# Optimization experiments

Hardware: AMD Instinct MI355X
Metric: run time of the kernel (lower is better)

The kernel has to match this reference:

```python
import jax, jax.numpy as jnp
import numpy as np

D_MODEL = 1024
D_STATE = 16
D_CONV = 4
EXPAND = 2
D_INNER = EXPAND * D_MODEL
DT_RANK = (D_MODEL + 15) // 16  # ceil(d_model/16) = 64
BATCH = 2
SEQLEN = 1024


def _causal_conv_silu(x, w, b):
    # x: (B, d_inner, L); w: (d_inner, 1, k) depthwise; causal left padding k-1
    k = w.shape[-1]
    y = jax.lax.conv_general_dilated(
        x, w, window_strides=(1,), padding=[(k - 1, 0)],
        dimension_numbers=("NCH", "OIH", "NCH"), feature_group_count=x.shape[1])
    return jax.nn.silu(y + b[None, :, None])


def _ssm_scan(dA, dBx):
    # h_t = dA_t * h_{t-1} + dBx_t, parallel associative scan over L (axis=2)
    def op(e1, e2):
        a1, b1 = e1
        a2, b2 = e2
        return (a1 * a2, a2 * b1 + b2)
    return jax.lax.associative_scan(op, (dA, dBx), axis=2)[1]


def _mamba_dir(xz, conv_w, conv_b, xproj_w, dtproj_w, dt_bias, A_log, Dp):
    d_inner = xz.shape[1] // 2
    x, z = xz[:, :d_inner], xz[:, d_inner:]
    u = _causal_conv_silu(x, conv_w, conv_b)                  # (B, d, L)
    x_dbl = jnp.einsum('bdl,kd->bkl', u, xproj_w)             # (B, dt_rank+2n, L)
    n = A_log.shape[1]
    r = dtproj_w.shape[1]
    delta = jnp.einsum('dr,brl->bdl', dtproj_w, x_dbl[:, :r])
    Bm = x_dbl[:, r:r + n]                                    # (B, n, L)
    Cm = x_dbl[:, r + n:]                                     # (B, n, L)
    delta = jax.nn.softplus(delta + dt_bias[None, :, None])
    A = -jnp.exp(A_log)                                       # (d, n)
    dA = jnp.exp(jnp.einsum('bdl,dn->bdln', delta, A))
    dBx = jnp.einsum('bdl,bnl,bdl->bdln', delta, Bm, u)
    h = _ssm_scan(dA, dBx)                                    # (B, d, L, n)
    y = jnp.einsum('bdln,bnl->bdl', h, Cm)
    y = y + Dp[None, :, None] * u
    return y * jax.nn.silu(z)


def setup_inputs() -> dict:
    key = jax.random.key(0)
    ks = jax.random.split(key, 16)
    s_in = 1.0 / np.sqrt(D_MODEL)
    s_x = 1.0 / np.sqrt(D_INNER)
    dt_std = DT_RANK ** -0.5

    def dt_bias_init(k):
        dt = jnp.exp(jax.random.uniform(k, (D_INNER,)) * (np.log(0.1) - np.log(0.001)) + np.log(0.001))
        dt = jnp.clip(dt, 1e-4, None)
        return dt + jnp.log(-jnp.expm1(-dt))  # inverse softplus

    A_log = jnp.log(jnp.tile(jnp.arange(1, D_STATE + 1, dtype=jnp.float32)[None, :], (D_INNER, 1)))
    inp = {
        'hidden_states': jax.random.normal(ks[0], (BATCH, SEQLEN, D_MODEL), jnp.float32),
        'in_proj_w': jax.random.normal(ks[1], (2 * D_INNER, D_MODEL), jnp.float32) * s_in,
        'conv_w': jax.random.normal(ks[2], (D_INNER, 1, D_CONV), jnp.float32) * 0.3,
        'conv_bias': jnp.zeros((D_INNER,), jnp.float32),
        'x_proj_w': jax.random.normal(ks[3], (DT_RANK + 2 * D_STATE, D_INNER), jnp.float32) * s_x,
        'dt_proj_w': jax.random.uniform(ks[4], (D_INNER, DT_RANK), jnp.float32, -dt_std, dt_std),
        'dt_proj_bias': dt_bias_init(ks[5]),
        'A_log': A_log,
        'D_skip': jnp.ones((D_INNER,), jnp.float32),
        'convb_w': jax.random.normal(ks[6], (D_INNER, 1, D_CONV), jnp.float32) * 0.3,
        'convb_bias': jnp.zeros((D_INNER,), jnp.float32),
        'x_proj_b_w': jax.random.normal(ks[7], (DT_RANK + 2 * D_STATE, D_INNER), jnp.float32) * s_x,
        'dt_proj_b_w': jax.random.uniform(ks[8], (D_INNER, DT_RANK), jnp.float32, -dt_std, dt_std),
        'dt_proj_b_bias': dt_bias_init(ks[9]),
        'A_b_log': A_log,
        'D_b_skip': jnp.ones((D_INNER,), jnp.float32),
        'out_proj_w': jax.random.normal(ks[10], (D_MODEL, D_INNER), jnp.float32) * s_x,
    }
    return inp


def reference(hidden_states, in_proj_w, conv_w, conv_bias, x_proj_w, dt_proj_w,
              dt_proj_bias, A_log, D_skip, convb_w, convb_bias, x_proj_b_w,
              dt_proj_b_w, dt_proj_b_bias, A_b_log, D_b_skip, out_proj_w):
    # in_proj (no bias): (B, 2*d_inner, L)
    xz = jnp.einsum('ed,bld->bel', in_proj_w, hidden_states)
    out_f = _mamba_dir(xz, conv_w, conv_bias, x_proj_w, dt_proj_w, dt_proj_bias, A_log, D_skip)
    out_b = _mamba_dir(xz[:, :, ::-1], convb_w, convb_bias, x_proj_b_w, dt_proj_b_w,
                       dt_proj_b_bias, A_b_log, D_b_skip)[:, :, ::-1]
    # if_divide_out=False: just sum then out_proj (no bias)
    return jnp.einsum('bdl,od->blo', out_f + out_b, out_proj_w)
```

## Files before the change

### kernel.cpp

```cpp
#include <hip/hip_runtime.h>
#include <math.h>


typedef _Float16 f16x8 __attribute__((ext_vector_type(8)));
typedef _Float16 f16x4 __attribute__((ext_vector_type(4)));
typedef float    f32x4 __attribute__((ext_vector_type(4)));

#define SCH 32
#define SCL 32

__device__ __forceinline__ void gload_lds16(const void* g, void* l) {
    __builtin_amdgcn_global_load_lds(
        (const __attribute__((address_space(1))) void*)g,
        (__attribute__((address_space(3))) void*)l, 16, 0, 0);
}

__device__ __forceinline__ float softplus_f(float x) {
    float e = __builtin_amdgcn_exp2f(-fabsf(x) * 1.44269504f);
    return fmaxf(x, 0.f) + __builtin_amdgcn_logf(1.f + e) * 0.69314718f;
}

template<int CTRL>
__device__ __forceinline__ float dpp_add(float x) {
    int s = __builtin_amdgcn_update_dpp(0, __builtin_bit_cast(int, x),
                                        CTRL, 0xF, 0xF, true);
    return x + __builtin_bit_cast(float, s);
}

template<int WMW, int WNW, int FM, int FN, typename CT>
__global__ __launch_bounds__(256)
void gemm_nt_f16(const _Float16* __restrict__ A, const _Float16* __restrict__ B,
                 CT* __restrict__ C, int K, int lda, int ldc,
                 long sA, long sB, long sC)
{
    constexpr int BM = WMW * FM * 16, BN = WNW * FN * 16;
    constexpr int ACH = BM / 8, NCH = (BM + BN) / 8;
    __shared__ __align__(16) _Float16 lds[(BM + BN) * 64];
    A += (long)blockIdx.z * sA;
    B += (long)blockIdx.z * sB;
    C += (long)blockIdx.z * sC;
    const int m0 = blockIdx.y * BM, n0 = blockIdx.x * BN;
    const int t = threadIdx.x, wid = t >> 6, lane = t & 63;
    const int wm = wid / WNW, wn = wid % WNW;
    const int srow = lane >> 3;
    const int skk  = ((lane & 7) ^ srow) * 8;

    f32x4 acc[FM][FN];
#pragma unroll
    for (int i = 0; i < FM; ++i)
#pragma unroll
        for (int j = 0; j < FN; ++j) acc[i][j] = (f32x4){0.f, 0.f, 0.f, 0.f};

    for (int k0 = 0; k0 < K; k0 += 64) {
#pragma unroll
        for (int c = wid; c < NCH; c += 4) {
            const _Float16* gp = (c < ACH)
                ? A + (long)(m0 + c * 8 + srow) * lda + k0 + skk
                : B + (long)(n0 + (c - ACH) * 8 + srow) * lda + k0 + skk;
            gload_lds16(gp, lds + c * 512);
        }
        __syncthreads();
#pragma unroll
        for (int kw = 0; kw < 2; ++kw) {
            f16x8 af[FM], bf[FN];
#pragma unroll
            for (int i = 0; i < FM; ++i) {
                int r = wm * FM * 16 + i * 16 + (lane & 15);
                af[i] = *(const f16x8*)(lds + r * 64 +
                        (((kw * 4 + (lane >> 4)) ^ (r & 7)) * 8));
            }
#pragma unroll
            for (int j = 0; j < FN; ++j) {
                int r = wn * FN * 16 + j * 16 + (lane & 15);
                bf[j] = *(const f16x8*)(lds + BM * 64 + r * 64 +
                        (((kw * 4 + (lane >> 4)) ^ (r & 7)) * 8));
            }
#pragma unroll
            for (int i = 0; i < FM; ++i)
#pragma unroll
                for (int j = 0; j < FN; ++j)
                    acc[i][j] = __builtin_amdgcn_mfma_f32_16x16x32_f16(
                        af[i], bf[j], acc[i][j], 0, 0, 0);
        }
        __syncthreads();
    }
#pragma unroll
    for (int i = 0; i < FM; ++i)
#pragma unroll
        for (int j = 0; j < FN; ++j) {
            int n = n0 + wn * FN * 16 + j * 16 + (lane & 15);
            int m = m0 + wm * FM * 16 + i * 16 + (lane >> 4) * 4;
            f32x4 v = acc[i][j];
            if constexpr (__is_same(CT, float)) {
                *(f32x4*)&C[(long)n * ldc + m] = v;
            } else {
                f16x4 h = {(_Float16)v.x, (_Float16)v.y, (_Float16)v.z, (_Float16)v.w};
                *(f16x4*)&C[(long)n * ldc + m] = h;
            }
        }
}

__global__ __launch_bounds__(256)
void oreduce_kernel(const float* __restrict__ p, float* __restrict__ out)
{
    int f = (blockIdx.x * 256 + threadIdx.x) * 4;
    f32x4 a = *(const f32x4*)(p + f);
    f32x4 b = *(const f32x4*)(p + 2097152 + f);
    *(f32x4*)(out + f) = a + b;
}

#define XP_SK 8
__global__ __launch_bounds__(256)
void xproj_f16_kernel(const _Float16* __restrict__ u16, const _Float16* __restrict__ xw16,
                      float* __restrict__ pb)
{
    __shared__ __align__(16) _Float16 Asw[128 * 64];
    __shared__ __align__(16) _Float16 Bsw[96 * 64];
    const int t = threadIdx.x, wid = t >> 6, lane = t & 63;
    const int wm = wid >> 1, wn = wid & 1;
    const int m0 = blockIdx.x * 128;
    const int sk = blockIdx.y, dirb = blockIdx.z;
    const _Float16* ub = u16 + (long)dirb * 2048 * 1024;
    const _Float16* Bw = xw16 + (long)(dirb >> 1) * 96 * 2048;
    const int srow = lane >> 3;
    const int skk  = ((lane & 7) ^ srow) * 8;
    const int lloc = (t & 31) * 4;
    const int kslt = t >> 5;

    f32x4 acc[4][3];
#pragma unroll
    for (int i = 0; i < 4; ++i)
#pragma unroll
        for (int j = 0; j < 3; ++j) acc[i][j] = (f32x4){0.f, 0.f, 0.f, 0.f};

    for (int ks = 0; ks < 2048 / XP_SK; ks += 64) {
        const int k0 = sk * (2048 / XP_SK) + ks;
#pragma unroll
        for (int c = wid; c < 12; c += 4)
            gload_lds16(Bw + (long)(c * 8 + srow) * 2048 + k0 + skk, Bsw + c * 512);
        _Float16 av[8][4];
#pragma unroll
        for (int kk = 0; kk < 8; ++kk) {
            f16x4 v = *(const f16x4*)&ub[(long)(k0 + kslt * 8 + kk) * 1024 + m0 + lloc];
            av[kk][0] = v[0]; av[kk][1] = v[1]; av[kk][2] = v[2]; av[kk][3] = v[3];
        }
#pragma unroll
        for (int q = 0; q < 4; ++q) {
            int l = lloc + q;
            f16x8 h = {av[0][q], av[1][q], av[2][q], av[3][q],
                       av[4][q], av[5][q], av[6][q], av[7][q]};
            *(f16x8*)(Asw + l * 64 + ((kslt ^ (l & 7)) * 8)) = h;
        }
        __syncthreads();
#pragma unroll
        for (int kw = 0; kw < 2; ++kw) {
            f16x8 af[4], bf[3];
#pragma unroll
            for (int i = 0; i < 4; ++i) {
                int r = wm * 64 + i * 16 + (lane & 15);
                af[i] = *(const f16x8*)(Asw + r * 64 +
                        (((kw * 4 + (lane >> 4)) ^ (r & 7)) * 8));
            }
#pragma unroll
            for (int j = 0; j < 3; ++j) {
                int r = wn * 48 + j * 16 + (lane & 15);
                bf[j] = *(const f16x8*)(Bsw + r * 64 +
                        (((kw * 4 + (lane >> 4)) ^ (r & 7)) * 8));
            }
#pragma unroll
            for (int i = 0; i < 4; ++i)
#pragma unroll
                for (int j = 0; j < 3; ++j)
                    acc[i][j] = __builtin_amdgcn_mfma_f32_16x16x32_f16(
                        af[i], bf[j], acc[i][j], 0, 0, 0);
        }
        __syncthreads();
    }
    float* Cp = pb + ((long)sk * 4 + dirb) * 96 * 1024;
#pragma unroll
    for (int i = 0; i < 4; ++i)
#pragma unroll
        for (int j = 0; j < 3; ++j) {
            int n = wn * 48 + j * 16 + (lane & 15);
            int m = m0 + wm * 64 + i * 16 + (lane >> 4) * 4;
            *(f32x4*)&Cp[(long)n * 1024 + m] = acc[i][j];
        }
}

__global__ __launch_bounds__(256)
void xreduce_kernel(const float* __restrict__ pb, float* __restrict__ xdbl)
{
    int f = (blockIdx.x * 256 + threadIdx.x) * 4;
    f32x4 s = (f32x4){0.f, 0.f, 0.f, 0.f};
#pragma unroll
    for (int sk = 0; sk < XP_SK; ++sk)
        s += *(const f32x4*)(pb + (long)sk * 393216 + f);
    *(f32x4*)(xdbl + f) = s;
}

__global__ __launch_bounds__(256)
void dtproj_f16_kernel(const float* __restrict__ xdbl, const _Float16* __restrict__ dw16,
                       const float* __restrict__ bcat, _Float16* __restrict__ delta16)
{
    __shared__ __align__(16) _Float16 Asw[128 * 64];
    __shared__ __align__(16) _Float16 Bsw[128 * 64];
    const int t = threadIdx.x, wid = t >> 6, lane = t & 63;
    const int wm = wid >> 1, wn = wid & 1;
    const int n0 = blockIdx.x * 128, m0 = blockIdx.y * 128;
    const int dirb = blockIdx.z, dir = dirb >> 1;
    const float* Xb = xdbl + (long)dirb * 96 * 1024;
    const _Float16* Bw = dw16 + (long)dir * 2048 * 64;
    const int srow = lane >> 3, skk = ((lane & 7) ^ srow) * 8;
    const int lloc = (t & 31) * 4, kslt = t >> 5;

#pragma unroll
    for (int c = wid; c < 16; c += 4)
        gload_lds16(Bw + (long)(n0 + c * 8 + srow) * 64 + skk, Bsw + c * 512);
    float av[8][4];
#pragma unroll
    for (int kk = 0; kk < 8; ++kk) {
        f32x4 v = *(const f32x4*)&Xb[(long)(kslt * 8 + kk) * 1024 + m0 + lloc];
        av[kk][0] = v.x; av[kk][1] = v.y; av[kk][2] = v.z; av[kk][3] = v.w;
    }
#pragma unroll
    for (int q = 0; q < 4; ++q) {
        int l = lloc + q;
        f16x8 h = {(_Float16)av[0][q], (_Float16)av[1][q], (_Float16)av[2][q],
                   (_Float16)av[3][q], (_Float16)av[4][q], (_Float16)av[5][q],
                   (_Float16)av[6][q], (_Float16)av[7][q]};
        *(f16x8*)(Asw + l * 64 + ((kslt ^ (l & 7)) * 8)) = h;
    }
    __syncthreads();

    f32x4 acc[4][4];
#pragma unroll
    for (int i = 0; i < 4; ++i)
#pragma unroll
        for (int j = 0; j < 4; ++j) acc[i][j] = (f32x4){0.f, 0.f, 0.f, 0.f};
#pragma unroll
    for (int kw = 0; kw < 2; ++kw) {
        f16x8 af[4], bf[4];
#pragma unroll
        for (int i = 0; i < 4; ++i) {
            int r = wm * 64 + i * 16 + (lane & 15);
            af[i] = *(const f16x8*)(Asw + r * 64 +
                    (((kw * 4 + (lane >> 4)) ^ (r & 7)) * 8));
        }
#pragma unroll
        for (int j = 0; j < 4; ++j) {
            int r = wn * 64 + j * 16 + (lane & 15);
            bf[j] = *(const f16x8*)(Bsw + r * 64 +
                    (((kw * 4 + (lane >> 4)) ^ (r & 7)) * 8));
        }
#pragma unroll
        for (int i = 0; i < 4; ++i)
#pragma unroll
            for (int j = 0; j < 4; ++j)
                acc[i][j] = __builtin_amdgcn_mfma_f32_16x16x32_f16(
                    af[i], bf[j], acc[i][j], 0, 0, 0);
    }
    _Float16* Dp = delta16 + (long)dirb * 2048 * 1024;
#pragma unroll
    for (int j = 0; j < 4; ++j) {
        int dd = n0 + wn * 64 + j * 16 + (lane & 15);
        float bm = bcat[dir * 2048 + dd];
#pragma unroll
        for (int i = 0; i < 4; ++i) {
            int m = m0 + wm * 64 + i * 16 + (lane >> 4) * 4;
            f32x4 v = acc[i][j];
            f16x4 o = {(_Float16)softplus_f(v.x + bm), (_Float16)softplus_f(v.y + bm),
                       (_Float16)softplus_f(v.z + bm), (_Float16)softplus_f(v.w + bm)};
            *(f16x4*)&Dp[(long)dd * 1024 + m] = o;
        }
    }
}

__global__ __launch_bounds__(256)
void setup_kernel(const float* __restrict__ hidden, const float* __restrict__ winp,
                  const float* __restrict__ woutp,
                  const float* __restrict__ xwf, const float* __restrict__ xwb,
                  const float* __restrict__ dwf, const float* __restrict__ dwb,
                  const float* __restrict__ bf,  const float* __restrict__ bb,
                  _Float16* __restrict__ H16, _Float16* __restrict__ Win16,
                  _Float16* __restrict__ Wout16,
                  _Float16* __restrict__ xw16, _Float16* __restrict__ dw16,
                  float* __restrict__ bcat)
{
    long i4 = ((long)blockIdx.x * 256 + threadIdx.x) * 4;
    auto cvt4 = [](const float* s) -> f16x4 {
        float4 v = *(const float4*)s;
        return (f16x4){(_Float16)v.x, (_Float16)v.y, (_Float16)v.z, (_Float16)v.w};
    };
    if (i4 < 4194304) *(f16x4*)(Win16 + i4) = cvt4(winp + i4);
    if (i4 < 2097152) {
        *(f16x4*)(H16 + i4)   = cvt4(hidden + i4);
        *(f16x4*)(Wout16 + i4) = cvt4(woutp + i4);
    }
    if (i4 < 196608) {
        *(f16x4*)(xw16 + i4)          = cvt4(xwf + i4);
        *(f16x4*)(xw16 + 196608 + i4) = cvt4(xwb + i4);
    }
    if (i4 < 131072) {
        *(f16x4*)(dw16 + i4)          = cvt4(dwf + i4);
        *(f16x4*)(dw16 + 131072 + i4) = cvt4(dwb + i4);
    }
    if (i4 < 2048) {
        *(float4*)(bcat + i4)        = *(const float4*)(bf + i4);
        *(float4*)(bcat + 2048 + i4) = *(const float4*)(bb + i4);
    }
}

__global__ __launch_bounds__(256)
void conv_silu_kernel(const _Float16* __restrict__ xz16,
                      const float* __restrict__ wf, const float* __restrict__ bf,
                      const float* __restrict__ wb, const float* __restrict__ bbk,
                      _Float16* __restrict__ u16)
{
    long idx = (long)blockIdx.x * 256 + threadIdx.x;
    int l = (int)(idx & 1023);
    long r = idx >> 10;
    int d = (int)(r & 2047);
    int b = (int)((r >> 11) & 1);
    int dir = (int)(r >> 12);
    const _Float16* x = xz16 + ((long)b * 4096 + d) * 1024;
    const float* w = dir ? wb : wf;
    float s = dir ? bbk[d] : bf[d];
    if (dir == 0) {
#pragma unroll
        for (int j = 0; j < 4; ++j) {
            int p = l - 3 + j;
            if (p >= 0) s = fmaf(w[d * 4 + j], (float)x[p], s);
        }
    } else {
#pragma unroll
        for (int j = 0; j < 4; ++j) {
            int src = l - 3 + j;
            if (src >= 0) s = fmaf(w[d * 4 + j], (float)x[1023 - src], s);
        }
    }
    u16[idx] = (_Float16)(s / (1.f + __builtin_amdgcn_exp2f(-s * 1.44269504f)));
}

__global__ __launch_bounds__(256)
void scan_p1_kernel(const _Float16* __restrict__ u16, const _Float16* __restrict__ delta16,
                    const float* __restrict__ xdbl,
                    const float* __restrict__ Alf, const float* __restrict__ Alb,
                    _Float16* __restrict__ hend16, _Float16* __restrict__ aprod16)
{
    __shared__ _Float16 sD[64][40], sU[64][40];
    __shared__ float sB[32][20];
    const int t = threadIdx.x, wid = t >> 6, lane = t & 63;
    const int nl = lane & 3;
    const int dloc = wid * 16 + (lane >> 2);
    const int dblk = blockIdx.x, chunk = blockIdx.y, dirb = blockIdx.z;
    const int d = dblk * 64 + dloc, dir = dirb >> 1;
    const int T0 = chunk * SCL;
    f32x4 Av = *(const f32x4*)((dir ? Alb : Alf) + d * 16 + nl * 4);
    float An2[4] = {-expf(Av.x) * 1.44269504f, -expf(Av.y) * 1.44269504f,
                    -expf(Av.z) * 1.44269504f, -expf(Av.w) * 1.44269504f};
    const _Float16* dp = delta16 + ((long)dirb * 2048 + dblk * 64) * 1024;
    const _Float16* up = u16    + ((long)dirb * 2048 + dblk * 64) * 1024;
    const float* Bp = xdbl + ((long)dirb * 96 + 64) * 1024;

    {
        int dd = t >> 2, q = t & 3;
        *(f16x8*)&sD[dd][q * 8] = *(const f16x8*)&dp[(long)dd * 1024 + T0 + q * 8];
        *(f16x8*)&sU[dd][q * 8] = *(const f16x8*)&up[(long)dd * 1024 + T0 + q * 8];
    }
#pragma unroll
    for (int rep = 0; rep < 2; ++rep) {
        int ii = rep * 256 + t;
        int n = ii >> 5, tt = ii & 31;
        sB[tt][n] = Bp[(long)n * 1024 + T0 + tt];
    }
    __syncthreads();

    float h[4] = {0.f, 0.f, 0.f, 0.f};
    float S = 0.f;
#pragma unroll 4
    for (int g = 0; g < 8; ++g) {
        f16x4 dlh = *(const f16x4*)&sD[dloc][g * 4];
        f16x4 uuh = *(const f16x4*)&sU[dloc][g * 4];
        float dls[4] = {(float)dlh[0], (float)dlh[1], (float)dlh[2], (float)dlh[3]};
        float uus[4] = {(float)uuh[0], (float)uuh[1], (float)uuh[2], (float)uuh[3]};
#pragma unroll
        for (int r4 = 0; r4 < 4; ++r4) {
            f32x4 Bv = *(const f32x4*)&sB[g * 4 + r4][nl * 4];
            float Bs[4] = {Bv.x, Bv.y, Bv.z, Bv.w};
            float dl = dls[r4], t1 = dl * uus[r4];
            S += dl;
#pragma unroll
            for (int r = 0; r < 4; ++r)
                h[r] = fmaf(__builtin_amdgcn_exp2f(dl * An2[r]), h[r], t1 * Bs[r]);
        }
    }
    long cb = (((long)dirb * SCH + chunk) * 2048 + d) * 16 + nl * 4;
    f16x4 he = {(_Float16)h[0], (_Float16)h[1], (_Float16)h[2], (_Float16)h[3]};
    f16x4 ap = {(_Float16)__builtin_amdgcn_exp2f(S * An2[0]),
                (_Float16)__builtin_amdgcn_exp2f(S * An2[1]),
                (_Float16)__builtin_amdgcn_exp2f(S * An2[2]),
                (_Float16)__builtin_amdgcn_exp2f(S * An2[3])};
    *(f16x4*)&hend16[cb]  = he;
    *(f16x4*)&aprod16[cb] = ap;
}

__global__ __launch_bounds__(256)
void scan_carry_kernel(const _Float16* __restrict__ hend16,
                       const _Float16* __restrict__ aprod16,
                       _Float16* __restrict__ hinit16)
{
    int f = blockIdx.x * 256 + threadIdx.x;
    int dn = f & 32767;
    int dirb = f >> 15;
    long base = (long)dirb * SCH * 32768 + dn;
    float hcur = 0.f;
#pragma unroll
    for (int c = 0; c < SCH; ++c) {
        hinit16[base + (long)c * 32768] = (_Float16)hcur;
        hcur = (float)hend16[base + (long)c * 32768]
             + (float)aprod16[base + (long)c * 32768] * hcur;
    }
}

__global__ __launch_bounds__(256)
void scan_p3_kernel(const _Float16* __restrict__ u16, const _Float16* __restrict__ delta16,
                    const float* __restrict__ xdbl,
                    const float* __restrict__ Alf, const float* __restrict__ Alb,
                    const float* __restrict__ Df, const float* __restrict__ Db,
                    const _Float16* __restrict__ hinit16, _Float16* __restrict__ y16)
{
    __shared__ _Float16 sD[64][40], sU[64][40];
    __shared__ float sB[32][20], sC[32][20];
    const int t = threadIdx.x, wid = t >> 6, lane = t & 63;
    const int nl = lane & 3;
    const int dloc = wid * 16 + (lane >> 2);
    const int dblk = blockIdx.x, chunk = blockIdx.y, dirb = blockIdx.z;
    const int d = dblk * 64 + dloc, dir = dirb >> 1;
    const int T0 = chunk * SCL;
    f32x4 Av = *(const f32x4*)((dir ? Alb : Alf) + d * 16 + nl * 4);
    float An2[4] = {-expf(Av.x) * 1.44269504f, -expf(Av.y) * 1.44269504f,
                    -expf(Av.z) * 1.44269504f, -expf(Av.w) * 1.44269504f};
    const float Dd = (dir ? Db : Df)[d];
    const _Float16* dp = delta16 + ((long)dirb * 2048 + dblk * 64) * 1024;
    const _Float16* up = u16    + ((long)dirb * 2048 + dblk * 64) * 1024;
    const float* Bp = xdbl + ((long)dirb * 96 + 64) * 1024;
    const float* Cp = xdbl + ((long)dirb * 96 + 80) * 1024;
    _Float16* yrow = y16 + ((long)dirb * 2048 + d) * 1024;

    {
        int dd = t >> 2, q = t & 3;
        *(f16x8*)&sD[dd][q * 8] = *(const f16x8*)&dp[(long)dd * 1024 + T0 + q * 8];
        *(f16x8*)&sU[dd][q * 8] = *(const f16x8*)&up[(long)dd * 1024 + T0 + q * 8];
    }
#pragma unroll
    for (int rep = 0; rep < 2; ++rep) {
        int ii = rep * 256 + t;
        int n = ii >> 5, tt = ii & 31;
        sB[tt][n] = Bp[(long)n * 1024 + T0 + tt];
        sC[tt][n] = Cp[(long)n * 1024 + T0 + tt];
    }
    long cb = (((long)dirb * SCH + chunk) * 2048 + d) * 16 + nl * 4;
    f16x4 h0v = *(const f16x4*)&hinit16[cb];
    float h[4] = {(float)h0v[0], (float)h0v[1], (float)h0v[2], (float)h0v[3]};
    const bool m[4] = {nl == 0, nl == 1, nl == 2, nl == 3};
    __syncthreads();

#pragma unroll 4
    for (int g = 0; g < 8; ++g) {
        f16x4 dlh = *(const f16x4*)&sD[dloc][g * 4];
        f16x4 uuh = *(const f16x4*)&sU[dloc][g * 4];
        float dls[4] = {(float)dlh[0], (float)dlh[1], (float)dlh[2], (float)dlh[3]};
        float uus[4] = {(float)uuh[0], (float)uuh[1], (float)uuh[2], (float)uuh[3]};
        float keep = 0.f;
#pragma unroll
        for (int r4 = 0; r4 < 4; ++r4) {
            f32x4 Bv = *(const f32x4*)&sB[g * 4 + r4][nl * 4];
            f32x4 Cv = *(const f32x4*)&sC[g * 4 + r4][nl * 4];
            float Bs[4] = {Bv.x, Bv.y, Bv.z, Bv.w};
            float Cs[4] = {Cv.x, Cv.y, Cv.z, Cv.w};
            float dl = dls[r4], uu = uus[r4];
            float t1 = dl * uu;
#pragma unroll
            for (int r = 0; r < 4; ++r)
                h[r] = fmaf(__builtin_amdgcn_exp2f(dl * An2[r]), h[r], t1 * Bs[r]);
            float p = h[0] * Cs[0];
            p = fmaf(h[1], Cs[1], p);
            p = fmaf(h[2], Cs[2], p);
            p = fmaf(h[3], Cs[3], p);
            p = dpp_add<0xB1>(p);
            p = dpp_add<0x4E>(p);
            float fy = fmaf(Dd, uu, p);
            keep = m[r4] ? fy : keep;
        }
        yrow[T0 + g * 4 + nl] = (_Float16)keep;
    }
}

__global__ __launch_bounds__(256)
void combine_T_kernel(const _Float16* __restrict__ xz16, const _Float16* __restrict__ y16,
                      _Float16* __restrict__ GT)
{
    __shared__ float Ls[64][65];
    const int d0 = blockIdx.x * 64, l0 = blockIdx.y * 64, b = blockIdx.z;
    const int t = threadIdx.x;
#pragma unroll
    for (int rep = 0; rep < 4; ++rep) {
        int i = rep * 256 + t;
        int dl = i >> 4;
        int lq = (i & 15) * 4;
        const _Float16* zp  = xz16 + ((long)b * 4096 + 2048 + d0 + dl) * 1024 + l0 + lq;
        const _Float16* yfp = y16 + ((long)(b)     * 2048 + d0 + dl) * 1024 + l0 + lq;
        const _Float16* ybp = y16 + ((long)(2 + b) * 2048 + d0 + dl) * 1024 + (1020 - l0 - lq);
        f16x4 vz = *(const f16x4*)zp;
        f16x4 vf = *(const f16x4*)yfp;
        f16x4 vb = *(const f16x4*)ybp;
        float zz[4]  = {(float)vz[0], (float)vz[1], (float)vz[2], (float)vz[3]};
        float ff[4]  = {(float)vf[0], (float)vf[1], (float)vf[2], (float)vf[3]};
        float bbv[4] = {(float)vb[3], (float)vb[2], (float)vb[1], (float)vb[0]};
#pragma unroll
        for (int qq = 0; qq < 4; ++qq) {
            float z = zz[qq];
            float sz = z / (1.f + __builtin_amdgcn_exp2f(-z * 1.44269504f));
            Ls[dl][lq + qq] = sz * (ff[qq] + bbv[qq]);
        }
    }
    __syncthreads();
#pragma unroll
    for (int rep = 0; rep < 4; ++rep) {
        int i = rep * 256 + t;
        int ll = i >> 4;
        int dq = (i & 15) * 4;
        f16x4 h = {(_Float16)Ls[dq][ll], (_Float16)Ls[dq + 1][ll],
                   (_Float16)Ls[dq + 2][ll], (_Float16)Ls[dq + 3][ll]};
        *(f16x4*)(GT + ((long)(b * 1024 + l0 + ll)) * 2048 + d0 + dq) = h;
    }
}

extern "C" void kernel_launch(void* const* d_in, const int* in_sizes, int n_in,
                              void* d_out, int out_size, void* d_ws, size_t ws_size,
                              hipStream_t stream)
{
    const float* hidden   = (const float*)d_in[0];
    const float* inproj_w = (const float*)d_in[1];
    const float* conv_w   = (const float*)d_in[2];
    const float* conv_b   = (const float*)d_in[3];
    const float* xproj_w  = (const float*)d_in[4];
    const float* dtproj_w = (const float*)d_in[5];
    const float* dt_bias  = (const float*)d_in[6];
    const float* A_log    = (const float*)d_in[7];
    const float* D_skip   = (const float*)d_in[8];
    const float* convb_w  = (const float*)d_in[9];
    const float* convb_b  = (const float*)d_in[10];
    const float* xprojb_w = (const float*)d_in[11];
    const float* dtprojb_w= (const float*)d_in[12];
    const float* dtb_bias = (const float*)d_in[13];
    const float* Ab_log   = (const float*)d_in[14];
    const float* Db_skip  = (const float*)d_in[15];
    const float* outproj_w= (const float*)d_in[16];
    float* out = (float*)d_out;

    float* ws    = (float*)d_ws;
    float* xz    = ws;
    float* u     = ws + 8388608;
    float* xdbl  = ws + 16777216;
    float* delta = ws + 17170432;
    float* y     = ws + 25559040;
    _Float16* xz16  = (_Float16*)xz;
    float*    opart = xz;
    _Float16* H16     = (_Float16*)u;
    _Float16* Win16   = (_Float16*)(u + 1048576);
    _Float16* u16     = (_Float16*)(u + 3145728);
    _Float16* Wout16  = (_Float16*)(u + 7340032);
    _Float16* hinit16 = (_Float16*)u;
    _Float16* delta16 = (_Float16*)delta;
    float*    xpb     = delta + 4194304;
    _Float16* GT      = (_Float16*)delta;
    _Float16* dw16  = (_Float16*)y;
    float*    bcat  = y + 131072;
    _Float16* xw16  = (_Float16*)(y + 135168);
    _Float16* hend16  = (_Float16*)y;
    _Float16* aprod16 = (_Float16*)(y + 2097152);
    _Float16* y16     = (_Float16*)y;

    hipLaunchKernelGGL(setup_kernel, dim3(4096), dim3(256), 0, stream,
        hidden, inproj_w, outproj_w, xproj_w, xprojb_w, dtproj_w, dtprojb_w,
        dt_bias, dtb_bias, H16, Win16, Wout16, xw16, dw16, bcat);

    hipLaunchKernelGGL((gemm_nt_f16<2, 2, 2, 4, _Float16>),
        dim3(32, 16, 2), dim3(256), 0, stream,
        H16, Win16, xz16, 1024, 1024, 1024, 1048576L, 0L, 4194304L);

    hipLaunchKernelGGL(conv_silu_kernel, dim3(32768), dim3(256), 0, stream,
        xz16, conv_w, conv_b, convb_w, convb_b, u16);

    hipLaunchKernelGGL(xproj_f16_kernel, dim3(8, XP_SK, 4), dim3(256), 0, stream,
        u16, xw16, xpb);
    hipLaunchKernelGGL(xreduce_kernel, dim3(384), dim3(256), 0, stream,
        xpb, xdbl);

    hipLaunchKernelGGL(dtproj_f16_kernel, dim3(16, 8, 4), dim3(256), 0, stream,
        xdbl, dw16, bcat, delta16);

    hipLaunchKernelGGL(scan_p1_kernel, dim3(32, SCH, 4), dim3(256), 0, stream,
        u16, delta16, xdbl, A_log, Ab_log, hend16, aprod16);
    hipLaunchKernelGGL(scan_carry_kernel, dim3(512), dim3(256), 0, stream,
        hend16, aprod16, hinit16);
    hipLaunchKernelGGL(scan_p3_kernel, dim3(32, SCH, 4), dim3(256), 0, stream,
        u16, delta16, xdbl, A_log, Ab_log, D_skip, Db_skip, hinit16, y16);

    hipLaunchKernelGGL(combine_T_kernel, dim3(32, 16, 2), dim3(256), 0, stream,
        xz16, y16, GT);

    hipLaunchKernelGGL((gemm_nt_f16<4, 1, 2, 4, float>),
        dim3(32, 8, 2), dim3(256), 0, stream,
        Wout16, GT, opart, 1024, 2048, 1024, 1024L, 1024L, 2097152L);

    hipLaunchKernelGGL(oreduce_kernel, dim3(2048), dim3(256), 0, stream,
        opart, out);
}
```

Before: 175.2 us.

## Fuse scan phase 3 with combine/transpose, processing both directions per block

Merges the third scan pass and the combine_T kernel: each block now runs the forward chunk and its mirrored backward chunk, keeps both y tiles in shared memory, applies the silu(z) gate and writes the transposed GT tile directly. This removes the y16 round-trip through global memory and one kernel launch. The cost is that each block does two serial scans, the grid is half as large, and shared-memory use grows, which may reduce occupancy and latency hiding.

```diff
diff --git a/kernel.cpp b/kernel.cpp
--- a/kernel.cpp
+++ b/kernel.cpp
@@ -423,116 +423,148 @@
 }
 
 __global__ __launch_bounds__(256)
-void scan_p3_kernel(const _Float16* __restrict__ u16, const _Float16* __restrict__ delta16,
-                    const float* __restrict__ xdbl,
-                    const float* __restrict__ Alf, const float* __restrict__ Alb,
-                    const float* __restrict__ Df, const float* __restrict__ Db,
-                    const _Float16* __restrict__ hinit16, _Float16* __restrict__ y16)
-{
-    __shared__ _Float16 sD[64][40], sU[64][40];
-    __shared__ float sB[32][20], sC[32][20];
+void scan_p3c_kernel(const _Float16* __restrict__ u16, const _Float16* __restrict__ delta16,
+                     const float* __restrict__ xdbl,
+                     const float* __restrict__ Alf, const float* __restrict__ Alb,
+                     const float* __restrict__ Df, const float* __restrict__ Db,
+                     const _Float16* __restrict__ hinit16,
+                     const _Float16* __restrict__ xz16,
+                     _Float16* __restrict__ GT)
+{
+    __shared__ _Float16 sDf[64][40], sUf[64][40], sDb[64][40], sUb[64][40];
+    __shared__ float sBf[32][20], sCf[32][20], sBb[32][20], sCb[32][20];
+    __shared__ _Float16 sYf[64][40], sYb[64][40];
     const int t = threadIdx.x, wid = t >> 6, lane = t & 63;
     const int nl = lane & 3;
     const int dloc = wid * 16 + (lane >> 2);
-    const int dblk = blockIdx.x, chunk = blockIdx.y, dirb = blockIdx.z;
-    const int d = dblk * 64 + dloc, dir = dirb >> 1;
-    const int T0 = chunk * SCL;
-    f32x4 Av = *(const f32x4*)((dir ? Alb : Alf) + d * 16 + nl * 4);
-    float An2[4] = {-expf(Av.x) * 1.44269504f, -expf(Av.y) * 1.44269504f,
-                    -expf(Av.z) * 1.44269504f, -expf(Av.w) * 1.44269504f};
-    const float Dd = (dir ? Db : Df)[d];
-    const _Float16* dp = delta16 + ((long)dirb * 2048 + dblk * 64) * 1024;
-    const _Float16* up = u16    + ((long)dirb * 2048 + dblk * 64) * 1024;
-    const float* Bp = xdbl + ((long)dirb * 96 + 64) * 1024;
-    const float* Cp = xdbl + ((long)dirb * 96 + 80) * 1024;
-    _Float16* yrow = y16 + ((long)dirb * 2048 + d) * 1024;
+    const int dblk = blockIdx.x, c = blockIdx.y, b = blockIdx.z;
+    const int d = dblk * 64 + dloc;
+    const int cB = SCH - 1 - c;
+    const int T0f = c * SCL, T0b = cB * SCL;
+    const int dirbF = b, dirbB = 2 + b;
+
+    f32x4 AvF = *(const f32x4*)(Alf + d * 16 + nl * 4);
+    f32x4 AvB = *(const f32x4*)(Alb + d * 16 + nl * 4);
+    float AnF[4] = {-expf(AvF.x) * 1.44269504f, -expf(AvF.y) * 1.44269504f,
+                    -expf(AvF.z) * 1.44269504f, -expf(AvF.w) * 1.44269504f};
+    float AnB[4] = {-expf(AvB.x) * 1.44269504f, -expf(AvB.y) * 1.44269504f,
+                    -expf(AvB.z) * 1.44269504f, -expf(AvB.w) * 1.44269504f};
+    const float DdF = Df[d], DdB = Db[d];
+    const _Float16* dpF = delta16 + ((long)dirbF * 2048 + dblk * 64) * 1024;
+    const _Float16* upF = u16    + ((long)dirbF * 2048 + dblk * 64) * 1024;
+    const _Float16* dpB = delta16 + ((long)dirbB * 2048 + dblk * 64) * 1024;
+    const _Float16* upB = u16    + ((long)dirbB * 2048 + dblk * 64) * 1024;
+    const float* BpF = xdbl + ((long)dirbF * 96 + 64) * 1024;
+    const float* CpF = xdbl + ((long)dirbF * 96 + 80) * 1024;
+    const float* BpB = xdbl + ((long)dirbB * 96 + 64) * 1024;
+    const float* CpB = xdbl + ((long)dirbB * 96 + 80) * 1024;
 
     {
         int dd = t >> 2, q = t & 3;
-        *(f16x8*)&sD[dd][q * 8] = *(const f16x8*)&dp[(long)dd * 1024 + T0 + q * 8];
-        *(f16x8*)&sU[dd][q * 8] = *(const f16x8*)&up[(long)dd * 1024 + T0 + q * 8];
+        *(f16x8*)&sDf[dd][q * 8] = *(const f16x8*)&dpF[(long)dd * 1024 + T0f + q * 8];
+        *(f16x8*)&sUf[dd][q * 8] = *(const f16x8*)&upF[(long)dd * 1024 + T0f + q * 8];
+        *(f16x8*)&sDb[dd][q * 8] = *(const f16x8*)&dpB[(long)dd * 1024 + T0b + q * 8];
+        *(f16x8*)&sUb[dd][q * 8] = *(const f16x8*)&upB[(long)dd * 1024 + T0b + q * 8];
     }
 #pragma unroll
     for (int rep = 0; rep < 2; ++rep) {
         int ii = rep * 256 + t;
         int n = ii >> 5, tt = ii & 31;
-        sB[tt][n] = Bp[(long)n * 1024 + T0 + tt];
-        sC[tt][n] = Cp[(long)n * 1024 + T0 + tt];
-    }
-    long cb = (((long)dirb * SCH + chunk) * 2048 + d) * 16 + nl * 4;
-    f16x4 h0v = *(const f16x4*)&hinit16[cb];
-    float h[4] = {(float)h0v[0], (float)h0v[1], (float)h0v[2], (float)h0v[3]};
+        sBf[tt][n] = BpF[(long)n * 1024 + T0f + tt];
+        sCf[tt][n] = CpF[(long)n * 1024 + T0f + tt];
+        sBb[tt][n] = BpB[(long)n * 1024 + T0b + tt];
+        sCb[tt][n] = CpB[(long)n * 1024 + T0b + tt];
+    }
+    long cbF = (((long)dirbF * SCH + c)  * 2048 + d) * 16 + nl * 4;
+    long cbB = (((long)dirbB * SCH + cB) * 2048 + d) * 16 + nl * 4;
+    f16x4 h0F = *(const f16x4*)&hinit16[cbF];
+    f16x4 h0B = *(const f16x4*)&hinit16[cbB];
     const bool m[4] = {nl == 0, nl == 1, nl == 2, nl == 3};
     __syncthreads();
 
+    {
+        float h[4] = {(float)h0F[0], (float)h0F[1], (float)h0F[2], (float)h0F[3]};
 #pragma unroll 4
-    for (int g = 0; g < 8; ++g) {
-        f16x4 dlh = *(const f16x4*)&sD[dloc][g * 4];
-        f16x4 uuh = *(const f16x4*)&sU[dloc][g * 4];
-        float dls[4] = {(float)dlh[0], (float)dlh[1], (float)dlh[2], (float)dlh[3]};
-        float uus[4] = {(float)uuh[0], (float)uuh[1], (float)uuh[2], (float)uuh[3]};
-        float keep = 0.f;
-#pragma unroll
-        for (int r4 = 0; r4 < 4; ++r4) {
-            f32x4 Bv = *(const f32x4*)&sB[g * 4 + r4][nl * 4];
-            f32x4 Cv = *(const f32x4*)&sC[g * 4 + r4][nl * 4];
-            float Bs[4] = {Bv.x, Bv.y, Bv.z, Bv.w};
-            float Cs[4] = {Cv.x, Cv.y, Cv.z, Cv.w};
-            float dl = dls[r4], uu = uus[r4];
-            float t1 = dl * uu;
-#pragma unroll
-            for (int r = 0; r < 4; ++r)
-                h[r] = fmaf(__builtin_amdgcn_exp2f(dl * An2[r]), h[r], t1 * Bs[r]);
-            float p = h[0] * Cs[0];
-            p = fmaf(h[1], Cs[1], p);
-            p = fmaf(h[2], Cs[2], p);
-            p = fmaf(h[3], Cs[3], p);
-            p = dpp_add<0xB1>(p);
-            p = dpp_add<0x4E>(p);
-            float fy = fmaf(Dd, uu, p);
-            keep = m[r4] ? fy : keep;
-        }
-        yrow[T0 + g * 4 + nl] = (_Float16)keep;
-    }
-}
-
-__global__ __launch_bounds__(256)
-void combine_T_kernel(const _Float16* __restrict__ xz16, const _Float16* __restrict__ y16,
-                      _Float16* __restrict__ GT)
-{
-    __shared__ float Ls[64][65];
-    const int d0 = blockIdx.x * 64, l0 = blockIdx.y * 64, b = blockIdx.z;
-    const int t = threadIdx.x;
-#pragma unroll
-    for (int rep = 0; rep < 4; ++rep) {
-        int i = rep * 256 + t;
-        int dl = i >> 4;
-        int lq = (i & 15) * 4;
-        const _Float16* zp  = xz16 + ((long)b * 4096 + 2048 + d0 + dl) * 1024 + l0 + lq;
-        const _Float16* yfp = y16 + ((long)(b)     * 2048 + d0 + dl) * 1024 + l0 + lq;
-        const _Float16* ybp = y16 + ((long)(2 + b) * 2048 + d0 + dl) * 1024 + (1020 - l0 - lq);
-        f16x4 vz = *(const f16x4*)zp;
-        f16x4 vf = *(const f16x4*)yfp;
-        f16x4 vb = *(const f16x4*)ybp;
-        float zz[4]  = {(float)vz[0], (float)vz[1], (float)vz[2], (float)vz[3]};
-        float ff[4]  = {(float)vf[0], (float)vf[1], (float)vf[2], (float)vf[3]};
-        float bbv[4] = {(float)vb[3], (float)vb[2], (float)vb[1], (float)vb[0]};
-#pragma unroll
-        for (int qq = 0; qq < 4; ++qq) {
-            float z = zz[qq];
+        for (int g = 0; g < 8; ++g) {
+            f16x4 dlh = *(const f16x4*)&sDf[dloc][g * 4];
+            f16x4 uuh = *(const f16x4*)&sUf[dloc][g * 4];
+            float dls[4] = {(float)dlh[0], (float)dlh[1], (float)dlh[2], (float)dlh[3]};
+            float uus[4] = {(float)uuh[0], (float)uuh[1], (float)uuh[2], (float)uuh[3]};
+            float keep = 0.f;
+#pragma unroll
+            for (int r4 = 0; r4 < 4; ++r4) {
+                f32x4 Bv = *(const f32x4*)&sBf[g * 4 + r4][nl * 4];
+                f32x4 Cv = *(const f32x4*)&sCf[g * 4 + r4][nl * 4];
+                float dl = dls[r4], uu = uus[r4], t1 = dl * uu;
+#pragma unroll
+                for (int r = 0; r < 4; ++r)
+                    h[r] = fmaf(__builtin_amdgcn_exp2f(dl * AnF[r]), h[r],
+                                t1 * ((const float*)&Bv)[r]);
+                float p = h[0] * Cv.x;
+                p = fmaf(h[1], Cv.y, p);
+                p = fmaf(h[2], Cv.z, p);
+                p = fmaf(h[3], Cv.w, p);
+                p = dpp_add<0xB1>(p);
+                p = dpp_add<0x4E>(p);
+                float fy = fmaf(DdF, uu, p);
+                keep = m[r4] ? fy : keep;
+            }
+            sYf[dloc][g * 4 + nl] = (_Float16)keep;
+        }
+    }
+    {
+        float h[4] = {(float)h0B[0], (float)h0B[1], (float)h0B[2], (float)h0B[3]};
+#pragma unroll 4
+        for (int g = 0; g < 8; ++g) {
+            f16x4 dlh = *(const f16x4*)&sDb[dloc][g * 4];
+            f16x4 uuh = *(const f16x4*)&sUb[dloc][g * 4];
+            float dls[4] = {(float)dlh[0], (float)dlh[1], (float)dlh[2], (float)dlh[3]};
+            float uus[4] = {(float)uuh[0], (float)uuh[1], (float)uuh[2], (float)uuh[3]};
+            float keep = 0.f;
+#pragma unroll
+            for (int r4 = 0; r4 < 4; ++r4) {
+                f32x4 Bv = *(const f32x4*)&sBb[g * 4 + r4][nl * 4];
+                f32x4 Cv = *(const f32x4*)&sCb[g * 4 + r4][nl * 4];
+                float dl = dls[r4], uu = uus[r4], t1 = dl * uu;
+#pragma unroll
+                for (int r = 0; r < 4; ++r)
+                    h[r] = fmaf(__builtin_amdgcn_exp2f(dl * AnB[r]), h[r],
+                                t1 * ((const float*)&Bv)[r]);
+                float p = h[0] * Cv.x;
+                p = fmaf(h[1], Cv.y, p);
+                p = fmaf(h[2], Cv.z, p);
+                p = fmaf(h[3], Cv.w, p);
+                p = dpp_add<0xB1>(p);
+                p = dpp_add<0x4E>(p);
+                float fy = fmaf(DdB, uu, p);
+                keep = m[r4] ? fy : keep;
+            }
+            sYb[dloc][31 - (g * 4 + nl)] = (_Float16)keep;
+        }
+    }
+    __syncthreads();
+
+    {
+        int dd = t >> 2, lq = (t & 3) * 8;
+        f16x8 vz = *(const f16x8*)&xz16[((long)b * 4096 + 2048 + dblk * 64 + dd) * 1024
+                                        + T0f + lq];
+#pragma unroll
+        for (int j = 0; j < 8; ++j) {
+            float z = (float)vz[j];
             float sz = z / (1.f + __builtin_amdgcn_exp2f(-z * 1.44269504f));
-            Ls[dl][lq + qq] = sz * (ff[qq] + bbv[qq]);
+            float g = sz * ((float)sYf[dd][lq + j] + (float)sYb[dd][lq + j]);
+            sDf[dd][lq + j] = (_Float16)g;
         }
     }
     __syncthreads();
-#pragma unroll
-    for (int rep = 0; rep < 4; ++rep) {
-        int i = rep * 256 + t;
-        int ll = i >> 4;
-        int dq = (i & 15) * 4;
-        f16x4 h = {(_Float16)Ls[dq][ll], (_Float16)Ls[dq + 1][ll],
-                   (_Float16)Ls[dq + 2][ll], (_Float16)Ls[dq + 3][ll]};
-        *(f16x4*)(GT + ((long)(b * 1024 + l0 + ll)) * 2048 + d0 + dq) = h;
+
+#pragma unroll
+    for (int rep = 0; rep < 2; ++rep) {
+        int ii = rep * 256 + t;
+        int ll = ii >> 4;
+        int dq = (ii & 15) * 4;
+        f16x4 h = {sDf[dq][ll], sDf[dq + 1][ll], sDf[dq + 2][ll], sDf[dq + 3][ll]};
+        *(f16x4*)(GT + ((long)(b * 1024 + T0f + ll)) * 2048 + dblk * 64 + dq) = h;
     }
 }
 
@@ -574,13 +606,12 @@
     _Float16* hinit16 = (_Float16*)u;
     _Float16* delta16 = (_Float16*)delta;
     float*    xpb     = delta + 4194304;
-    _Float16* GT      = (_Float16*)delta;
     _Float16* dw16  = (_Float16*)y;
     float*    bcat  = y + 131072;
     _Float16* xw16  = (_Float16*)(y + 135168);
     _Float16* hend16  = (_Float16*)y;
     _Float16* aprod16 = (_Float16*)(y + 2097152);
-    _Float16* y16     = (_Float16*)y;
+    _Float16* GT      = (_Float16*)y;
 
     hipLaunchKernelGGL(setup_kernel, dim3(4096), dim3(256), 0, stream,
         hidden, inproj_w, outproj_w, xproj_w, xprojb_w, dtproj_w, dtprojb_w,
@@ -605,11 +636,8 @@
         u16, delta16, xdbl, A_log, Ab_log, hend16, aprod16);
     hipLaunchKernelGGL(scan_carry_kernel, dim3(512), dim3(256), 0, stream,
         hend16, aprod16, hinit16);
-    hipLaunchKernelGGL(scan_p3_kernel, dim3(32, SCH, 4), dim3(256), 0, stream,
-        u16, delta16, xdbl, A_log, Ab_log, D_skip, Db_skip, hinit16, y16);
-
-    hipLaunchKernelGGL(combine_T_kernel, dim3(32, 16, 2), dim3(256), 0, stream,
-        xz16, y16, GT);
+    hipLaunchKernelGGL(scan_p3c_kernel, dim3(32, SCH, 2), dim3(256), 0, stream,
+        u16, delta16, xdbl, A_log, Ab_log, D_skip, Db_skip, hinit16, xz16, GT);
 
     hipLaunchKernelGGL((gemm_nt_f16<4, 1, 2, 4, float>),
         dim3(32, 8, 2), dim3(256), 0, stream,
```

Measured after the change: 173.4 us. About the same (-1.0%).
